# Performance work log

Hardware: AMD Instinct MI355X
Metric: run time of the kernel (lower is better)

## Reference

```python
import jax, jax.numpy as jnp
import numpy as np


def conv3x3(x, w):
    # x: [B,C,H,W], w: [O,I,3,3], stride 1, pad 1, no bias
    return jax.lax.conv_general_dilated(
        x, w, window_strides=(1, 1), padding=[(1, 1), (1, 1)],
        dimension_numbers=("NCHW", "OIHW", "NCHW"))


def deform_conv2d(x, offset, w):
    """torchvision-style DeformConv2d: k=3, stride=1, pad=1, dilation=1,
    1 offset group, no bias. x:[B,C,H,W], offset:[B,18,H,W] (dy,dx pairs
    per kernel tap, k = kh*3+kw), w:[O,C,3,3]. Zero padding outside."""
    B, C, H, W = x.shape
    K = 9
    dy = offset[:, 0::2]  # [B,9,H,W]
    dx = offset[:, 1::2]
    kh = (jnp.arange(K) // 3 - 1).astype(x.dtype)[None, :, None, None]
    kw = (jnp.arange(K) % 3 - 1).astype(x.dtype)[None, :, None, None]
    hh = jnp.arange(H, dtype=x.dtype)[None, None, :, None]
    ww = jnp.arange(W, dtype=x.dtype)[None, None, None, :]
    py = hh + kh + dy  # sampling y coord, [B,9,H,W]
    px = ww + kw + dx
    y0 = jnp.floor(py)
    x0 = jnp.floor(px)
    wy = py - y0
    wx = px - x0
    x_hwc = jnp.transpose(x, (0, 2, 3, 1))  # [B,H,W,C]
    b_idx = jnp.arange(B)[:, None, None, None]

    def gather(yi, xi):
        valid = (yi >= 0) & (yi <= H - 1) & (xi >= 0) & (xi <= W - 1)
        yc = jnp.clip(yi, 0, H - 1).astype(jnp.int32)
        xc = jnp.clip(xi, 0, W - 1).astype(jnp.int32)
        v = x_hwc[b_idx, yc, xc]  # [B,9,H,W,C]
        return v * valid[..., None].astype(x.dtype)

    v00 = gather(y0, x0)
    v01 = gather(y0, x0 + 1)
    v10 = gather(y0 + 1, x0)
    v11 = gather(y0 + 1, x0 + 1)
    wy = wy[..., None]
    wx = wx[..., None]
    sampled = (v00 * (1 - wy) * (1 - wx) + v01 * (1 - wy) * wx
               + v10 * wy * (1 - wx) + v11 * wy * wx)  # [B,9,H,W,C]
    wk = w.reshape(w.shape[0], w.shape[1], K)  # [O,C,9]
    return jnp.einsum("bkhwc,ock->bohw", sampled, wk)


def setup_inputs() -> dict:
    key = jax.random.key(0)
    ks = jax.random.split(key, 6)
    B, C, H, W = 2, 128, 128, 128
    s = 0.05  # small init so learned offsets stay in a realistic range
    return {
        "input_features": jax.random.normal(ks[0], (B, C, H, W), jnp.float32),
        "reference_features": jax.random.normal(ks[1], (B, C, H, W), jnp.float32),
        "w_est1": jax.random.normal(ks[2], (C, 2 * C, 3, 3), jnp.float32) * s,
        "w_est2": jax.random.normal(ks[3], (C, C, 3, 3), jnp.float32) * s,
        "w_off": jax.random.normal(ks[4], (18, C, 3, 3), jnp.float32) * s,
        "w_def": jax.random.normal(ks[5], (C, C, 3, 3), jnp.float32) * s,
    }


def reference(input_features, reference_features, w_est1, w_est2, w_off, w_def):
    # concat input+reference features along channel dim
    feat = jnp.concatenate([input_features, reference_features], axis=1)  # [B,2C,H,W]
    # dynamic offset estimator: 2-layer 3x3 conv stack 2C->C->C with ReLU
    est = jax.nn.relu(conv3x3(feat, w_est1))
    est = jax.nn.relu(conv3x3(est, w_est2))
    # offset head: C -> 2*9 offsets per pixel
    offset = conv3x3(est, w_off)  # [B,18,H,W]
    # deformable conv over the reference features
    return deform_conv2d(reference_features, offset, w_def)
```

## Files before the change

kernel.cpp:

```cpp
#include <hip/hip_runtime.h>

typedef _Float16 f16;
typedef __attribute__((ext_vector_type(8))) _Float16 f16x8;
typedef __attribute__((ext_vector_type(4))) float f32x4;
typedef __attribute__((ext_vector_type(4))) int i32x4;


__device__ __forceinline__ void pack_conv(const float* __restrict__ src, f16* __restrict__ dst,
                                          long idx, int C) {
  int ci3 = idx & 7;
  int g = (idx >> 3) & 3;
  long t = idx >> 5;
  int o = (int)(t & 63); t >>= 6;
  int kx = (int)(t % 3); t /= 3;
  int nb = (int)(t & 1); t >>= 1;
  int nkc = C >> 5;
  int cc = (int)(t % nkc);
  int ky = (int)(t / nkc);
  int og = nb * 64 + o;
  int c = (cc << 5) + ((g ^ ((o >> 1) & 3)) << 3) + ci3;
  dst[idx] = (f16)src[(((size_t)og * C + c) * 3 + ky) * 3 + kx];
}

__device__ __forceinline__ void halo_zero(f16* __restrict__ buf, long e) {
  int c = (int)(e & 127);
  long t = e >> 7;
  int b = (int)(t / 516);
  int p = (int)(t % 516);
  int y, x;
  if (p < 130)      { y = 0;   x = p; }
  else if (p < 260) { y = 129; x = p - 130; }
  else if (p < 388) { x = 0;   y = p - 259; }
  else              { x = 129; y = p - 387; }
  buf[((size_t)(b * 130 + y) * 130 + x) * 128 + c] = (f16)0.f;
}

__global__ __launch_bounds__(256) void init_k(const float* __restrict__ x, const float* __restrict__ ref,
                                              const float* __restrict__ w1, const float* __restrict__ w2,
                                              const float* __restrict__ woff, const float* __restrict__ wdef,
                                              f16* __restrict__ W1p, f16* __restrict__ W2p,
                                              f16* __restrict__ Woffp, f16* __restrict__ Wdefp,
                                              f16* __restrict__ xP, f16* __restrict__ refP,
                                              f16* __restrict__ est1, f16* __restrict__ est2) {
  __shared__ __align__(16) f16 T[64][40];
  int tid = threadIdx.x;
  if (blockIdx.x < 4096) {
    int bi = blockIdx.x;
    int row = bi & 255, wseg = (bi >> 8) & 1, chunk = bi >> 9;
    int b = row >> 7, h = row & 127;
    int w0 = wseg * 64;
    const float* src = (chunk < 4) ? x : ref;
    f16* dstp = (chunk < 4) ? xP : refP;
    int c0 = (chunk & 3) * 32;
#pragma unroll
    for (int i = 0; i < 2; ++i) {
      int idx = tid + i * 256;
      int c = idx >> 4, g = idx & 15;
      const float4 v = *(const float4*)(src + (((size_t)(b * 128 + c0 + c)) * 128 + h) * 128 + w0 + g * 4);
      T[g * 4 + 0][c] = (f16)v.x;
      T[g * 4 + 1][c] = (f16)v.y;
      T[g * 4 + 2][c] = (f16)v.z;
      T[g * 4 + 3][c] = (f16)v.w;
    }
    __syncthreads();
    int w = tid >> 2, g = tid & 3;
    f16x8 o = *(const f16x8*)&T[w][g * 8];
    *(f16x8*)(dstp + ((size_t)(b * 130 + h + 1) * 130 + w0 + w + 1) * 128 + c0 + g * 8) = o;
    return;
  }
  long idx = (long)(blockIdx.x - 4096) * 256 + tid;
  if (idx < 294912) { pack_conv(w1, W1p, idx, 256); return; }
  idx -= 294912;
  if (idx < 147456) { pack_conv(w2, W2p, idx, 128); return; }
  idx -= 147456;
  if (idx < 36864) {
    int ci3 = (int)(idx & 7);
    int g = (int)((idx >> 3) & 3);
    int o = (int)((idx >> 5) & 31);
    int t2 = (int)(idx >> 10);
    int kx = t2 % 3; t2 /= 3;
    int cc = t2 & 3, ky = t2 >> 2;
    int c = (cc << 5) + ((g ^ ((o >> 1) & 3)) << 3) + ci3;
    Woffp[idx] = (o < 18) ? (f16)woff[(((size_t)o * 128 + c) * 3 + ky) * 3 + kx] : (f16)0.f;
    return;
  }
  idx -= 36864;
  if (idx < 147456) {
    int j = (int)(idx & 7);
    int ln = (int)((idx >> 3) & 63);
    int ofr = (int)((idx >> 9) & 7);
    int cc = (int)((idx >> 12) & 3);
    int t = (int)(idx >> 14);
    int o = ofr * 16 + (ln & 15);
    int c = cc * 32 + (ln >> 4) * 8 + j;
    Wdefp[idx] = (f16)wdef[(((size_t)o * 128 + c) * 3 + t / 3) * 3 + t % 3];
    return;
  }
  idx -= 147456;
  if (idx < 132096) { halo_zero(xP, idx); return; }
  idx -= 132096;
  if (idx < 132096) { halo_zero(refP, idx); return; }
  idx -= 132096;
  if (idx < 132096) { halo_zero(est1, idx); return; }
  idx -= 132096;
  if (idx < 132096) halo_zero(est2, idx);
}

template <int NKC>
__global__ __launch_bounds__(256, 2) void conv_k(const f16* __restrict__ src0,
                                                 const f16* __restrict__ src1,
                                                 const f16* __restrict__ Wp,
                                                 f16* __restrict__ dst) {
  constexpr int S = 3 * NKC;
  const int j = blockIdx.x;
  const int xcd = j & 7, ji = j >> 3;
  const int row = xcd * 32 + (ji & 31);
  const int nb = ji >> 5;
  const int b = row >> 7, h = row & 127;
  __shared__ __align__(16) f16 As[3][130][32];
  __shared__ __align__(16) f16 Bs[3][3][64][32];
  const int tid = threadIdx.x;
  const int lane = tid & 63, wave = tid >> 6;
  const int l16 = lane & 15, quad = lane >> 4;
  const int wmB = wave * 32;
  f32x4 acc[2][4] = {};

  i32x4 ra0, ra1, ra2, rb0, rb1, rb2;

  auto stage_load = [&](int s) {
    int ky = s / NKC, cc = s % NKC;
    const f16* sp = (NKC == 8 && cc >= 4) ? src1 : src0;
    int c0 = (NKC == 8 ? (cc & 3) : cc) * 32;
    const f16* abase = sp + ((size_t)(b * 130 + h + ky) * 130) * 128 + c0;
    {
      int ch = tid;
      int xx = ch >> 2, g = ch & 3;
      ra0 = *(const i32x4*)(abase + (size_t)xx * 128 + ((g ^ ((xx >> 1) & 3)) << 3));
    }
    {
      int ch = 256 + tid;
      int xx = ch >> 2, g = ch & 3;
      ra1 = *(const i32x4*)(abase + (size_t)xx * 128 + ((g ^ ((xx >> 1) & 3)) << 3));
    }
    if (tid < 8) {
      int ch = 512 + tid;
      int xx = ch >> 2, g = ch & 3;
      ra2 = *(const i32x4*)(abase + (size_t)xx * 128 + ((g ^ ((xx >> 1) & 3)) << 3));
    }
    const f16* bbase = Wp + (size_t)((ky * NKC + cc) * 2 + nb) * (3 * 64 * 32);
    rb0 = *(const i32x4*)(bbase + (size_t)tid * 8);
    rb1 = *(const i32x4*)(bbase + (size_t)(256 + tid) * 8);
    rb2 = *(const i32x4*)(bbase + (size_t)(512 + tid) * 8);
  };
  auto stage_write = [&](int buf) {
    *(i32x4*)((char*)&As[buf][0][0] + tid * 16) = ra0;
    *(i32x4*)((char*)&As[buf][0][0] + (256 + tid) * 16) = ra1;
    if (tid < 8)
      *(i32x4*)((char*)&As[buf][0][0] + (512 + tid) * 16) = ra2;
    *(i32x4*)((char*)&Bs[buf][0][0][0] + tid * 16) = rb0;
    *(i32x4*)((char*)&Bs[buf][0][0][0] + (256 + tid) * 16) = rb1;
    *(i32x4*)((char*)&Bs[buf][0][0][0] + (512 + tid) * 16) = rb2;
  };

  stage_load(0);
  stage_write(0);
  stage_load(1);
  __syncthreads();
  for (int s = 0; s < S; ++s) {
    const int buf = s % 3;
#pragma unroll
    for (int kx = 0; kx < 3; ++kx) {
      f16x8 bf[4];
#pragma unroll
      for (int j2 = 0; j2 < 4; ++j2) {
        int o = j2 * 16 + l16;
        bf[j2] = *(const f16x8*)&Bs[buf][kx][o][(quad ^ ((o >> 1) & 3)) << 3];
      }
#pragma unroll
      for (int i = 0; i < 2; ++i) {
        int xx = wmB + i * 16 + l16 + kx;
        f16x8 a = *(const f16x8*)&As[buf][xx][(quad ^ ((xx >> 1) & 3)) << 3];
#pragma unroll
        for (int j2 = 0; j2 < 4; ++j2)
          acc[i][j2] = __builtin_amdgcn_mfma_f32_16x16x32_f16(a, bf[j2], acc[i][j2], 0, 0, 0);
      }
    }
    if (s + 1 < S) stage_write((s + 1) % 3);
    if (s + 2 < S) stage_load(s + 2);
    __syncthreads();
  }
#pragma unroll
  for (int i = 0; i < 2; ++i)
#pragma unroll
    for (int j2 = 0; j2 < 4; ++j2) {
      int o = nb * 64 + j2 * 16 + l16;
#pragma unroll
      for (int rr = 0; rr < 4; ++rr) {
        int m = wmB + i * 16 + quad * 4 + rr;
        float v = fmaxf(acc[i][j2][rr], 0.f);
        dst[((size_t)(b * 130 + h + 1) * 130 + m + 1) * 128 + o] = (f16)v;
      }
    }
}

__global__ __launch_bounds__(256, 2) void conv_off_k(const f16* __restrict__ src,
                                                     const f16* __restrict__ Wp,
                                                     float* __restrict__ dst) {
  const int j = blockIdx.x;
  const int row = (j & 7) * 32 + (j >> 3);
  const int b = row >> 7, h = row & 127;
  __shared__ __align__(16) f16 As[3][130][32];
  __shared__ __align__(16) f16 Bs[3][3][32][32];
  const int tid = threadIdx.x;
  const int lane = tid & 63, wave = tid >> 6;
  const int l16 = lane & 15, quad = lane >> 4;
  const int wmB = wave * 32;
  f32x4 acc[2][2] = {};

  i32x4 ra0, ra1, ra2, rb0, rb1;

  auto stage_load = [&](int s) {
    int ky = s >> 2, cc = s & 3;
    const f16* abase = src + ((size_t)(b * 130 + h + ky) * 130) * 128 + cc * 32;
    {
      int ch = tid;
      int xx = ch >> 2, g = ch & 3;
      ra0 = *(const i32x4*)(abase + (size_t)xx * 128 + ((g ^ ((xx >> 1) & 3)) << 3));
    }
    {
      int ch = 256 + tid;
      int xx = ch >> 2, g = ch & 3;
      ra1 = *(const i32x4*)(abase + (size_t)xx * 128 + ((g ^ ((xx >> 1) & 3)) << 3));
    }
    if (tid < 8) {
      int ch = 512 + tid;
      int xx = ch >> 2, g = ch & 3;
      ra2 = *(const i32x4*)(abase + (size_t)xx * 128 + ((g ^ ((xx >> 1) & 3)) << 3));
    }
    const f16* bbase = Wp + (size_t)(ky * 4 + cc) * (3 * 32 * 32);
    rb0 = *(const i32x4*)(bbase + (size_t)tid * 8);
    if (tid < 128) rb1 = *(const i32x4*)(bbase + (size_t)(256 + tid) * 8);
  };
  auto stage_write = [&](int buf) {
    *(i32x4*)((char*)&As[buf][0][0] + tid * 16) = ra0;
    *(i32x4*)((char*)&As[buf][0][0] + (256 + tid) * 16) = ra1;
    if (tid < 8)
      *(i32x4*)((char*)&As[buf][0][0] + (512 + tid) * 16) = ra2;
    *(i32x4*)((char*)&Bs[buf][0][0][0] + tid * 16) = rb0;
    if (tid < 128)
      *(i32x4*)((char*)&Bs[buf][0][0][0] + (256 + tid) * 16) = rb1;
  };

  stage_load(0);
  stage_write(0);
  stage_load(1);
  __syncthreads();
  for (int s = 0; s < 12; ++s) {
    const int buf = s % 3;
#pragma unroll
    for (int kx = 0; kx < 3; ++kx) {
      f16x8 bf[2];
#pragma unroll
      for (int j2 = 0; j2 < 2; ++j2) {
        int o = j2 * 16 + l16;
        bf[j2] = *(const f16x8*)&Bs[buf][kx][o][(quad ^ ((o >> 1) & 3)) << 3];
      }
#pragma unroll
      for (int i = 0; i < 2; ++i) {
        int xx = wmB + i * 16 + l16 + kx;
        f16x8 a = *(const f16x8*)&As[buf][xx][(quad ^ ((xx >> 1) & 3)) << 3];
#pragma unroll
        for (int j2 = 0; j2 < 2; ++j2)
          acc[i][j2] = __builtin_amdgcn_mfma_f32_16x16x32_f16(a, bf[j2], acc[i][j2], 0, 0, 0);
      }
    }
    if (s + 1 < 12) stage_write((s + 1) % 3);
    if (s + 2 < 12) stage_load(s + 2);
    __syncthreads();
  }
#pragma unroll
  for (int i = 0; i < 2; ++i)
#pragma unroll
    for (int j2 = 0; j2 < 2; ++j2)
#pragma unroll
      for (int rr = 0; rr < 4; ++rr) {
        int m = wmB + i * 16 + quad * 4 + rr;
        int o = j2 * 16 + l16;
        dst[((size_t)row * 128 + m) * 32 + o] = acc[i][j2][rr];
      }
}

__global__ __launch_bounds__(256, 2) void deform_k(const f16* __restrict__ refP,
                                                   const float* __restrict__ offb,
                                                   const f16* __restrict__ Wdefp,
                                                   float* __restrict__ out) {
  const int j = blockIdx.x;
  const int xcd = j & 7, ji = j >> 3;
  const int row = xcd * 32 + (ji & 31);
  const int tile = ji >> 5;
  const int b = row >> 7, h = row & 127;
  __shared__ __align__(16) f16 Ss[2][64][128];
  __shared__ int4 meta[9][64];
  const int tid = threadIdx.x;
  const int lane = tid & 63, wave = tid >> 6;
  const int l16 = lane & 15, quad = lane >> 4;

  for (int e = tid; e < 576; e += 256) {
    int t = e >> 6, p = e & 63;
    int wg = tile * 64 + p;
    const float2 d = *(const float2*)(offb + ((size_t)row * 128 + wg) * 32 + 2 * t);
    float py = (float)(h + t / 3 - 1) + d.x;
    float px = (float)(wg + t % 3 - 1) + d.y;
    float fy = floorf(py), fx = floorf(px);
    meta[t][p] = make_int4((int)fy, (int)fx, __float_as_int(py - fy), __float_as_int(px - fx));
  }

  const int sp_p = tid >> 2, sp_cg = tid & 3;
  f16x8 v00[4], v01[4], v10[4], v11[4];
  f16 h00, h01, h10, h11;

  auto sample_issue = [&](int t) {
    int4 mt = meta[t][sp_p];
    int yp = mt.x + 1, xp = mt.y + 1;
    float wy = __int_as_float(mt.z), wx = __int_as_float(mt.w);
    bool y0v = (unsigned)yp < 130u, y1v = (unsigned)(yp + 1) < 130u;
    bool x0v = (unsigned)xp < 130u, x1v = (unsigned)(xp + 1) < 130u;
    int cy0 = y0v ? yp : 0, cy1 = y1v ? yp + 1 : 0;
    int cx0 = x0v ? xp : 0, cx1 = x1v ? xp + 1 : 0;
    float u0 = (1.f - wy) * (y0v ? 1.f : 0.f), u1 = wy * (y1v ? 1.f : 0.f);
    float s0 = (1.f - wx) * (x0v ? 1.f : 0.f), s1 = wx * (x1v ? 1.f : 0.f);
    h00 = (f16)(u0 * s0); h01 = (f16)(u0 * s1);
    h10 = (f16)(u1 * s0); h11 = (f16)(u1 * s1);
    const size_t bb = (size_t)b * 130;
    const f16* p00 = refP + ((bb + cy0) * 130 + cx0) * 128 + sp_cg * 32;
    const f16* p01 = refP + ((bb + cy0) * 130 + cx1) * 128 + sp_cg * 32;
    const f16* p10 = refP + ((bb + cy1) * 130 + cx0) * 128 + sp_cg * 32;
    const f16* p11 = refP + ((bb + cy1) * 130 + cx1) * 128 + sp_cg * 32;
#pragma unroll
    for (int q = 0; q < 4; ++q) {
      v00[q] = *(const f16x8*)(p00 + q * 8);
      v01[q] = *(const f16x8*)(p01 + q * 8);
      v10[q] = *(const f16x8*)(p10 + q * 8);
      v11[q] = *(const f16x8*)(p11 + q * 8);
    }
  };
  auto sample_finish = [&](int buf) {
#pragma unroll
    for (int q = 0; q < 4; ++q) {
      f16x8 rb = v00[q] * h00 + v01[q] * h01 + v10[q] * h10 + v11[q] * h11;
      int c = sp_cg * 4 + q;
      *(f16x8*)&Ss[buf][sp_p][(c ^ (sp_p & 7)) << 3] = rb;
    }
  };

  f32x4 acc[2][4] = {};
  __syncthreads();
  sample_issue(0);
  sample_finish(0);
  __syncthreads();
  for (int t = 0; t < 9; ++t) {
    f16x8 af[4][2];
#pragma unroll
    for (int cc = 0; cc < 4; ++cc)
#pragma unroll
      for (int i = 0; i < 2; ++i)
        af[cc][i] = *(const f16x8*)(Wdefp +
            ((((size_t)t * 4 + cc) * 8 + wave * 2 + i) * 64 + lane) * 8);
    if (t < 8) sample_issue(t + 1);
    const int buf = t & 1;
#pragma unroll
    for (int cc = 0; cc < 4; ++cc) {
      f16x8 bf[4];
#pragma unroll
      for (int j2 = 0; j2 < 4; ++j2) {
        int p = j2 * 16 + l16;
        bf[j2] = *(const f16x8*)&Ss[buf][p][((cc * 4 + quad) ^ (p & 7)) << 3];
      }
#pragma unroll
      for (int i = 0; i < 2; ++i)
#pragma unroll
        for (int j2 = 0; j2 < 4; ++j2)
          acc[i][j2] = __builtin_amdgcn_mfma_f32_16x16x32_f16(af[cc][i], bf[j2], acc[i][j2], 0, 0, 0);
    }
    if (t < 8) sample_finish((t + 1) & 1);
    __syncthreads();
  }
#pragma unroll
  for (int i = 0; i < 2; ++i)
#pragma unroll
    for (int rr = 0; rr < 4; ++rr) {
      int o = wave * 32 + i * 16 + quad * 4 + rr;
#pragma unroll
      for (int j2 = 0; j2 < 4; ++j2) {
        int wg = tile * 64 + j2 * 16 + l16;
        out[((size_t)(b * 128 + o) * 128 + h) * 128 + wg] = acc[i][j2][rr];
      }
    }
}

extern "C" void kernel_launch(void* const* d_in, const int* in_sizes, int n_in,
                              void* d_out, int out_size, void* d_ws, size_t ws_size,
                              hipStream_t stream) {
  const float* x = (const float*)d_in[0];
  const float* ref = (const float*)d_in[1];
  const float* w1 = (const float*)d_in[2];
  const float* w2 = (const float*)d_in[3];
  const float* woff = (const float*)d_in[4];
  const float* wdef = (const float*)d_in[5];
  float* out = (float*)d_out;
  char* ws = (char*)d_ws;
  f16* xP = (f16*)(ws + 0);
  f16* refP = (f16*)(ws + 8652800);
  f16* est1 = (f16*)(ws + 17305600);
  f16* est2 = (f16*)(ws + 25958400);
  float* offb = (float*)(ws + 34611200);
  f16* W1p = (f16*)(ws + 38805504);
  f16* W2p = (f16*)(ws + 39395328);
  f16* Woffp = (f16*)(ws + 39690240);
  f16* Wdefp = (f16*)(ws + 39763968);

  init_k<<<dim3(8608), 256, 0, stream>>>(x, ref, w1, w2, woff, wdef,
                                         W1p, W2p, Woffp, Wdefp, xP, refP, est1, est2);
  conv_k<8><<<dim3(512), 256, 0, stream>>>(xP, refP, W1p, est1);
  conv_k<4><<<dim3(512), 256, 0, stream>>>(est1, est1, W2p, est2);
  conv_off_k<<<dim3(256), 256, 0, stream>>>(est2, Woffp, offb);
  deform_k<<<dim3(512), 256, 0, stream>>>(refP, offb, Wdefp, out);
}
```

Before: 161.6 us.

## Fuse offset-head conv into deformable conv kernel via shared-memory staging

Removes the separate conv_off_k launch and computes the 18-channel offset conv for each 64-pixel tile inside deform_k. The results go into a shared float buffer instead of a global offset array. This saves one kernel launch and the global write and read of the offsets. In exchange, deform_k uses more shared memory, aliasing the conv staging buffers onto the sampling buffer, and gains a 12-stage MFMA prologue before sampling. The halo rows of est2 are now loaded redundantly by neighbouring tiles.

Measured after the change: 161.3 us. Within noise of the previous version (-0.2%).

```diff
diff --git a/kernel.cpp b/kernel.cpp
--- a/kernel.cpp
+++ b/kernel.cpp
@@ -203,95 +203,9 @@
     }
 }
 
-__global__ __launch_bounds__(256, 2) void conv_off_k(const f16* __restrict__ src,
-                                                     const f16* __restrict__ Wp,
-                                                     float* __restrict__ dst) {
-  const int j = blockIdx.x;
-  const int row = (j & 7) * 32 + (j >> 3);
-  const int b = row >> 7, h = row & 127;
-  __shared__ __align__(16) f16 As[3][130][32];
-  __shared__ __align__(16) f16 Bs[3][3][32][32];
-  const int tid = threadIdx.x;
-  const int lane = tid & 63, wave = tid >> 6;
-  const int l16 = lane & 15, quad = lane >> 4;
-  const int wmB = wave * 32;
-  f32x4 acc[2][2] = {};
-
-  i32x4 ra0, ra1, ra2, rb0, rb1;
-
-  auto stage_load = [&](int s) {
-    int ky = s >> 2, cc = s & 3;
-    const f16* abase = src + ((size_t)(b * 130 + h + ky) * 130) * 128 + cc * 32;
-    {
-      int ch = tid;
-      int xx = ch >> 2, g = ch & 3;
-      ra0 = *(const i32x4*)(abase + (size_t)xx * 128 + ((g ^ ((xx >> 1) & 3)) << 3));
-    }
-    {
-      int ch = 256 + tid;
-      int xx = ch >> 2, g = ch & 3;
-      ra1 = *(const i32x4*)(abase + (size_t)xx * 128 + ((g ^ ((xx >> 1) & 3)) << 3));
-    }
-    if (tid < 8) {
-      int ch = 512 + tid;
-      int xx = ch >> 2, g = ch & 3;
-      ra2 = *(const i32x4*)(abase + (size_t)xx * 128 + ((g ^ ((xx >> 1) & 3)) << 3));
-    }
-    const f16* bbase = Wp + (size_t)(ky * 4 + cc) * (3 * 32 * 32);
-    rb0 = *(const i32x4*)(bbase + (size_t)tid * 8);
-    if (tid < 128) rb1 = *(const i32x4*)(bbase + (size_t)(256 + tid) * 8);
-  };
-  auto stage_write = [&](int buf) {
-    *(i32x4*)((char*)&As[buf][0][0] + tid * 16) = ra0;
-    *(i32x4*)((char*)&As[buf][0][0] + (256 + tid) * 16) = ra1;
-    if (tid < 8)
-      *(i32x4*)((char*)&As[buf][0][0] + (512 + tid) * 16) = ra2;
-    *(i32x4*)((char*)&Bs[buf][0][0][0] + tid * 16) = rb0;
-    if (tid < 128)
-      *(i32x4*)((char*)&Bs[buf][0][0][0] + (256 + tid) * 16) = rb1;
-  };
-
-  stage_load(0);
-  stage_write(0);
-  stage_load(1);
-  __syncthreads();
-  for (int s = 0; s < 12; ++s) {
-    const int buf = s % 3;
-#pragma unroll
-    for (int kx = 0; kx < 3; ++kx) {
-      f16x8 bf[2];
-#pragma unroll
-      for (int j2 = 0; j2 < 2; ++j2) {
-        int o = j2 * 16 + l16;
-        bf[j2] = *(const f16x8*)&Bs[buf][kx][o][(quad ^ ((o >> 1) & 3)) << 3];
-      }
-#pragma unroll
-      for (int i = 0; i < 2; ++i) {
-        int xx = wmB + i * 16 + l16 + kx;
-        f16x8 a = *(const f16x8*)&As[buf][xx][(quad ^ ((xx >> 1) & 3)) << 3];
-#pragma unroll
-        for (int j2 = 0; j2 < 2; ++j2)
-          acc[i][j2] = __builtin_amdgcn_mfma_f32_16x16x32_f16(a, bf[j2], acc[i][j2], 0, 0, 0);
-      }
-    }
-    if (s + 1 < 12) stage_write((s + 1) % 3);
-    if (s + 2 < 12) stage_load(s + 2);
-    __syncthreads();
-  }
-#pragma unroll
-  for (int i = 0; i < 2; ++i)
-#pragma unroll
-    for (int j2 = 0; j2 < 2; ++j2)
-#pragma unroll
-      for (int rr = 0; rr < 4; ++rr) {
-        int m = wmB + i * 16 + quad * 4 + rr;
-        int o = j2 * 16 + l16;
-        dst[((size_t)row * 128 + m) * 32 + o] = acc[i][j2][rr];
-      }
-}
-
 __global__ __launch_bounds__(256, 2) void deform_k(const f16* __restrict__ refP,
-                                                   const float* __restrict__ offb,
+                                                   const f16* __restrict__ est2,
+                                                   const f16* __restrict__ Woffp,
                                                    const f16* __restrict__ Wdefp,
                                                    float* __restrict__ out) {
   const int j = blockIdx.x;
@@ -299,18 +213,81 @@
   const int row = xcd * 32 + (ji & 31);
   const int tile = ji >> 5;
   const int b = row >> 7, h = row & 127;
-  __shared__ __align__(16) f16 Ss[2][64][128];
+  __shared__ __align__(16) char smem[32768];
+  __shared__ __align__(16) float offs[64][32];
   __shared__ int4 meta[9][64];
+  f16 (*Ss)[64][128] = (f16(*)[64][128])smem;
+  f16 (*As3)[66][32] = (f16(*)[66][32])smem;
+  f16 (*Bs3)[3][32][32] = (f16(*)[3][32][32])(smem + 12672);
   const int tid = threadIdx.x;
   const int lane = tid & 63, wave = tid >> 6;
   const int l16 = lane & 15, quad = lane >> 4;
+  const int x0 = tile * 64;
+
+  {
+    i32x4 ra0, ra1, rb0, rb1;
+    auto sl = [&](int s) {
+      int ky = s >> 2, cc = s & 3;
+      const f16* abase = est2 + (((size_t)(b * 130 + h + ky)) * 130 + x0) * 128 + cc * 32;
+      {
+        int ch = tid;
+        int xx = ch >> 2, g = ch & 3;
+        ra0 = *(const i32x4*)(abase + (size_t)xx * 128 + ((g ^ ((xx >> 1) & 3)) << 3));
+      }
+      if (tid < 8) {
+        int ch = 256 + tid;
+        int xx = ch >> 2, g = ch & 3;
+        ra1 = *(const i32x4*)(abase + (size_t)xx * 128 + ((g ^ ((xx >> 1) & 3)) << 3));
+      }
+      const f16* bbase = Woffp + (size_t)(ky * 4 + cc) * (3 * 32 * 32);
+      rb0 = *(const i32x4*)(bbase + (size_t)tid * 8);
+      if (tid < 128) rb1 = *(const i32x4*)(bbase + (size_t)(256 + tid) * 8);
+    };
+    auto sw = [&](int buf) {
+      *(i32x4*)((char*)&As3[buf][0][0] + tid * 16) = ra0;
+      if (tid < 8)
+        *(i32x4*)((char*)&As3[buf][0][0] + (256 + tid) * 16) = ra1;
+      *(i32x4*)((char*)&Bs3[buf][0][0][0] + tid * 16) = rb0;
+      if (tid < 128)
+        *(i32x4*)((char*)&Bs3[buf][0][0][0] + (256 + tid) * 16) = rb1;
+    };
+    f32x4 oacc[2] = {};
+    sl(0); sw(0); sl(1);
+    __syncthreads();
+    for (int s = 0; s < 12; ++s) {
+      const int buf = s % 3;
+#pragma unroll
+      for (int kx = 0; kx < 3; ++kx) {
+        f16x8 bf[2];
+#pragma unroll
+        for (int j2 = 0; j2 < 2; ++j2) {
+          int o = j2 * 16 + l16;
+          bf[j2] = *(const f16x8*)&Bs3[buf][kx][o][(quad ^ ((o >> 1) & 3)) << 3];
+        }
+        int xx = wave * 16 + l16 + kx;
+        f16x8 a = *(const f16x8*)&As3[buf][xx][(quad ^ ((xx >> 1) & 3)) << 3];
+#pragma unroll
+        for (int j2 = 0; j2 < 2; ++j2)
+          oacc[j2] = __builtin_amdgcn_mfma_f32_16x16x32_f16(a, bf[j2], oacc[j2], 0, 0, 0);
+      }
+      if (s + 1 < 12) sw((s + 1) % 3);
+      if (s + 2 < 12) sl(s + 2);
+      __syncthreads();
+    }
+#pragma unroll
+    for (int j2 = 0; j2 < 2; ++j2)
+#pragma unroll
+      for (int rr = 0; rr < 4; ++rr)
+        offs[wave * 16 + quad * 4 + rr][j2 * 16 + l16] = oacc[j2][rr];
+  }
+  __syncthreads();
 
   for (int e = tid; e < 576; e += 256) {
     int t = e >> 6, p = e & 63;
     int wg = tile * 64 + p;
-    const float2 d = *(const float2*)(offb + ((size_t)row * 128 + wg) * 32 + 2 * t);
-    float py = (float)(h + t / 3 - 1) + d.x;
-    float px = (float)(wg + t % 3 - 1) + d.y;
+    float dy = offs[p][2 * t], dx = offs[p][2 * t + 1];
+    float py = (float)(h + t / 3 - 1) + dy;
+    float px = (float)(wg + t % 3 - 1) + dx;
     float fy = floorf(py), fx = floorf(px);
     meta[t][p] = make_int4((int)fy, (int)fx, __float_as_int(py - fy), __float_as_int(px - fx));
   }
@@ -413,16 +390,14 @@
   f16* refP = (f16*)(ws + 8652800);
   f16* est1 = (f16*)(ws + 17305600);
   f16* est2 = (f16*)(ws + 25958400);
-  float* offb = (float*)(ws + 34611200);
-  f16* W1p = (f16*)(ws + 38805504);
-  f16* W2p = (f16*)(ws + 39395328);
-  f16* Woffp = (f16*)(ws + 39690240);
-  f16* Wdefp = (f16*)(ws + 39763968);
+  f16* W1p = (f16*)(ws + 34611200);
+  f16* W2p = (f16*)(ws + 35201024);
+  f16* Woffp = (f16*)(ws + 35495936);
+  f16* Wdefp = (f16*)(ws + 35569664);
 
   init_k<<<dim3(8608), 256, 0, stream>>>(x, ref, w1, w2, woff, wdef,
                                          W1p, W2p, Woffp, Wdefp, xP, refP, est1, est2);
   conv_k<8><<<dim3(512), 256, 0, stream>>>(xP, refP, W1p, est1);
   conv_k<4><<<dim3(512), 256, 0, stream>>>(est1, est1, W2p, est2);
-  conv_off_k<<<dim3(256), 256, 0, stream>>>(est2, Woffp, offb);
-  deform_k<<<dim3(512), 256, 0, stream>>>(refP, offb, Wdefp, out);
-}
+  deform_k<<<dim3(512), 256, 0, stream>>>(refP, est2, Woffp, Wdefp, out);
+}
```
